# Kernel tuning notes

Hardware: AMD Instinct MI355X
Metric: run time of the kernel (lower is better)

## Reference

```python
import jax, jax.numpy as jnp
import numpy as np

B, C1, D1, C2, D2 = 128, 1152, 8, 10, 16
ROUTING_ITERS = 3


def squash(s, axis=-1, eps=1e-8):
    # squash(s) = (|s|^2 / (1+|s|^2)) * s / sqrt(|s|^2 + eps)
    sq = jnp.sum(s * s, axis=axis, keepdims=True)
    return (sq / (1.0 + sq)) * s / jnp.sqrt(sq + eps)


def setup_inputs() -> dict:
    key = jax.random.key(0)
    k1, k2, k3 = jax.random.split(key, 3)
    inputs = jax.random.normal(k1, (B, C1 * D1), dtype=jnp.float32)
    # W: (caps1, caps2, d2, d1), truncated normal stddev=0.1 (leading batch-1 dim dropped)
    W = jax.random.truncated_normal(k2, -2.0, 2.0, (C1, C2, D2, D1), dtype=jnp.float32) * 0.1
    # routing bias: (1, 1, caps2, d2)
    bias = jax.random.normal(k3, (1, 1, C2, D2), dtype=jnp.float32) * 0.1
    return {"inputs": inputs, "W": W, "bias": bias}


def reference(inputs, W, bias):
    b = inputs.shape[0]
    # PrimaryCaps: reshape to [B, C1, D1] then squash over the capsule dim (axis=-2 of
    # the original [B, C1, 1, D1, 1] tensor == D1 here)
    prim = squash(inputs.reshape(b, C1, D1), axis=-1)
    # DigitalCaps (fast): u_hat[b,i,j,:] = W[i,j] @ prim[b,i]  -> [B, C1, C2, D2]
    u_hat = jnp.einsum('cjdk,bck->bcjd', W, prim)
    u_stop = jax.lax.stop_gradient(u_hat)
    raw = jnp.zeros((b, C1, C2, 1), dtype=inputs.dtype)
    v = None
    for r in range(ROUTING_ITERS):
        u = u_hat if r == ROUTING_ITERS - 1 else u_stop
        c = jax.nn.softmax(raw, axis=2)                      # softmax over output caps
        s = jnp.sum(c * u, axis=1, keepdims=True) + bias     # [B, 1, C2, D2]
        v = squash(s, axis=-1)                               # squash over D2 (orig axis=-2)
        if r != ROUTING_ITERS - 1:
            # agreement: sum over D2 of u * v (v broadcasts over C1)
            raw = raw + jnp.sum(u * v, axis=-1, keepdims=True)
    # original returns [B, 1, C2, D2, 1]
    return v[..., None]
```

## Files before the change

### kernel.cpp

```cpp
#include <hip/hip_runtime.h>
#include <hip/hip_fp16.h>

#define BATCH 128
#define NC1   1152
#define ND1   8
#define NC2   10
#define ND2   16
#define SDIM  (NC2 * ND2)

#define CB 16
#define BB 32

#define NQ   6
#define QCAP (NC1 / NQ)
#define CPGP (QCAP / 32)

__device__ __forceinline__ unsigned pack_h2(float a, float b) {
    __half2 h = __floats2half2_rn(a, b);
    return *reinterpret_cast<unsigned*>(&h);
}
__device__ __forceinline__ float2 unpack_h2(unsigned v) {
    __half2 h = *reinterpret_cast<__half2*>(&v);
    return __half22float2(h);
}
__device__ __forceinline__ unsigned pmul_h2(unsigned a, unsigned b) {
    __half2 ha = *reinterpret_cast<__half2*>(&a);
    __half2 hb = *reinterpret_cast<__half2*>(&b);
    __half2 r = __hmul2(ha, hb);
    return *reinterpret_cast<unsigned*>(&r);
}
__device__ __forceinline__ unsigned padd_h2(unsigned a, unsigned b) {
    __half2 ha = *reinterpret_cast<__half2*>(&a);
    __half2 hb = *reinterpret_cast<__half2*>(&b);
    __half2 r = __hadd2(ha, hb);
    return *reinterpret_cast<unsigned*>(&r);
}

template<int CTRL>
__device__ __forceinline__ unsigned dpp_mov(unsigned v) {
    return (unsigned)__builtin_amdgcn_mov_dpp((int)v, CTRL, 0xF, 0xF, true);
}
__device__ __forceinline__ unsigned row_reduce_h2(unsigned t2) {
    t2 = padd_h2(t2, dpp_mov<0x128>(t2));
    t2 = padd_h2(t2, dpp_mov<0x124>(t2));
    t2 = padd_h2(t2, dpp_mov<0x122>(t2));
    t2 = padd_h2(t2, dpp_mov<0x121>(t2));
    return t2;
}

__global__ void caps_zero(float* __restrict__ s0) {
    s0[blockIdx.x * 256 + threadIdx.x] = 0.0f;
}

__global__ __launch_bounds__(256, 1) void caps_uhat(
    const float* __restrict__ x,
    const float* __restrict__ W,
    unsigned* __restrict__ u_ws,
    float* __restrict__ s0)
{
    const int cb  = blockIdx.x;
    const int bb  = blockIdx.y;
    const int tid = threadIdx.x;
    const int cl  = tid >> 4;
    const int d   = tid & 15;
    const int wl  = tid & 63;

    __shared__ float prim[BB][CB][ND1];

    for (int i = tid; i < BB * CB; i += 256) {
        const int b = i >> 4, c = i & 15;
        const float* xr = x + ((size_t)(bb * BB + b) * NC1 + (cb * CB + c)) * ND1;
        float4 a0 = *(const float4*)(xr);
        float4 a1 = *(const float4*)(xr + 4);
        float sq = a0.x*a0.x + a0.y*a0.y + a0.z*a0.z + a0.w*a0.w
                 + a1.x*a1.x + a1.y*a1.y + a1.z*a1.z + a1.w*a1.w;
        float g = (sq / (1.0f + sq)) * rsqrtf(sq + 1e-8f);
        prim[b][c][0] = a0.x * g; prim[b][c][1] = a0.y * g;
        prim[b][c][2] = a0.z * g; prim[b][c][3] = a0.w * g;
        prim[b][c][4] = a1.x * g; prim[b][c][5] = a1.y * g;
        prim[b][c][6] = a1.z * g; prim[b][c][7] = a1.w * g;
    }
    __syncthreads();

    const int c_glob = cb * CB + cl;
    float w[NC2][ND1];
    #pragma unroll
    for (int j = 0; j < NC2; ++j) {
        const float* Wr = W + (((size_t)c_glob * NC2 + j) * ND2 + d) * ND1;
        float4 w0 = *(const float4*)(Wr);
        float4 w1 = *(const float4*)(Wr + 4);
        w[j][0] = w0.x; w[j][1] = w0.y; w[j][2] = w0.z; w[j][3] = w0.w;
        w[j][4] = w1.x; w[j][5] = w1.y; w[j][6] = w1.z; w[j][7] = w1.w;
    }

    for (int k = 0; k < BB; ++k) {
        const int b = (k + cb) & (BB - 1);
        const int bglob = bb * BB + b;
        float p[ND1];
        #pragma unroll
        for (int kk = 0; kk < ND1; ++kk) p[kk] = prim[b][cl][kk];

        unsigned* ur = u_ws + ((size_t)bglob * 5 * NC1 + c_glob) * 16 + d;
        #pragma unroll
        for (int jp = 0; jp < 5; ++jp) {
            float u0 = 0.f, u1 = 0.f;
            #pragma unroll
            for (int kk = 0; kk < ND1; ++kk) {
                u0 += w[2*jp  ][kk] * p[kk];
                u1 += w[2*jp+1][kk] * p[kk];
            }
            unsigned pk = pack_h2(u0, u1);
            ur[(size_t)jp * (NC1 * 16)] = pk;
            pk = padd_h2(pk, (unsigned)__shfl_xor((int)pk, 16));
            pk = padd_h2(pk, (unsigned)__shfl_xor((int)pk, 32));
            if (wl < 16) {
                float2 f = unpack_h2(pk);
                atomicAdd(&s0[(size_t)bglob * SDIM + (2*jp)   * 16 + d], f.x);
                atomicAdd(&s0[(size_t)bglob * SDIM + (2*jp+1) * 16 + d], f.y);
            }
        }
    }
}

__global__ __launch_bounds__(512, 1) void caps_pass(
    const unsigned* __restrict__ u_ws,
    const float* __restrict__ s0,
    const float* __restrict__ spart_in,
    const float* __restrict__ bias,
    float* __restrict__ spart_out,
    int mode)
{
    const int bx   = blockIdx.x;
    const int b    = bx / NQ;
    const int q    = bx % NQ;
    const int tid  = threadIdx.x;
    const int grp  = tid >> 4;
    const int d    = tid & 15;
    const int wave = tid >> 6;

    __shared__ float vl[SDIM];
    __shared__ float sred[8][SDIM];

    const unsigned* ub = u_ws + (size_t)b * 5 * NC1 * 16 + d;
    const int c0 = q * QCAP + grp;
    unsigned uo[CPGP][5];
    #pragma unroll
    for (int i = 0; i < CPGP; ++i) {
        const int c = c0 + i * 32;
        #pragma unroll
        for (int jp = 0; jp < 5; ++jp)
            uo[i][jp] = ub[(size_t)jp * (NC1 * 16) + (size_t)c * 16];
    }

    if (tid < SDIM) {
        float bv = bias[tid];
        float s_a = 0.1f * s0[(size_t)b * SDIM + tid] + bv;
        float qa = s_a * s_a;
        qa += __shfl_xor(qa, 1); qa += __shfl_xor(qa, 2);
        qa += __shfl_xor(qa, 4); qa += __shfl_xor(qa, 8);
        float v = (qa / (1.0f + qa)) * rsqrtf(qa + 1e-8f) * s_a;
        if (mode == 1) {
            float s_b = bv;
            #pragma unroll
            for (int qq = 0; qq < NQ; ++qq)
                s_b += spart_in[((size_t)b * NQ + qq) * SDIM + tid];
            float qb = s_b * s_b;
            qb += __shfl_xor(qb, 1); qb += __shfl_xor(qb, 2);
            qb += __shfl_xor(qb, 4); qb += __shfl_xor(qb, 8);
            v += (qb / (1.0f + qb)) * rsqrtf(qb + 1e-8f) * s_b;
        }
        vl[tid] = v;
    }
    __syncthreads();

    unsigned vsf[5];
    #pragma unroll
    for (int jp = 0; jp < 5; ++jp)
        vsf[jp] = pack_h2(vl[(2*jp)*16 + d], vl[(2*jp+1)*16 + d]);

    float sp[NC2];
    #pragma unroll
    for (int j = 0; j < NC2; ++j) sp[j] = 0.0f;

    #pragma unroll
    for (int i = 0; i < CPGP; ++i) {
        float u[NC2], r[NC2];
        #pragma unroll
        for (int jp = 0; jp < 5; ++jp) {
            float2 f = unpack_h2(uo[i][jp]);
            u[2*jp] = f.x; u[2*jp+1] = f.y;
            unsigned t2 = row_reduce_h2(pmul_h2(uo[i][jp], vsf[jp]));
            float2 rr = unpack_h2(t2);
            r[2*jp] = rr.x; r[2*jp+1] = rr.y;
        }
        float ssum = 0.0f;
        #pragma unroll
        for (int j = 0; j < NC2; ++j) { r[j] = __expf(r[j]); ssum += r[j]; }
        float inv = 1.0f / ssum;
        #pragma unroll
        for (int j = 0; j < NC2; ++j) sp[j] += (r[j] * inv) * u[j];
    }

    #pragma unroll
    for (int j = 0; j < NC2; ++j) {
        sp[j] += __shfl_xor(sp[j], 16);
        sp[j] += __shfl_xor(sp[j], 32);
    }
    if ((tid & 63) < 16) {
        #pragma unroll
        for (int j = 0; j < NC2; ++j) sred[wave][j * 16 + d] = sp[j];
    }
    __syncthreads();
    if (tid < SDIM) {
        float acc = 0.0f;
        #pragma unroll
        for (int w = 0; w < 8; ++w) acc += sred[w][tid];
        spart_out[((size_t)b * NQ + q) * SDIM + tid] = acc;
    }
}

__global__ void caps_comb2(const float* __restrict__ spart,
                           const float* __restrict__ bias,
                           float* __restrict__ out) {
    const int b = blockIdx.x, tid = threadIdx.x;
    if (tid >= SDIM) return;
    float s = bias[tid];
    #pragma unroll
    for (int q = 0; q < NQ; ++q)
        s += spart[((size_t)b * NQ + q) * SDIM + tid];
    float sq = s * s;
    sq += __shfl_xor(sq, 1); sq += __shfl_xor(sq, 2);
    sq += __shfl_xor(sq, 4); sq += __shfl_xor(sq, 8);
    out[(size_t)b * SDIM + tid] = (sq / (1.0f + sq)) * rsqrtf(sq + 1e-8f) * s;
}

__global__ __launch_bounds__(1024) void caps_fused(
    const float* __restrict__ x, const float* __restrict__ W,
    const float* __restrict__ bias, float* __restrict__ out)
{
    const int b    = blockIdx.x;
    const int tid  = threadIdx.x;
    const int grp  = tid >> 4;
    const int d    = tid & 15;
    const int wave = tid >> 6;
    const int lane = tid & 63;

    __shared__ float prim[NC1][ND1];
    __shared__ float sred[16][SDIM];
    __shared__ float vbuf[SDIM];

    const float* xb = x + (size_t)b * (NC1 * ND1);
    for (int c = tid; c < NC1; c += 1024) {
        float4 a0 = *(const float4*)(xb + c * 8);
        float4 a1 = *(const float4*)(xb + c * 8 + 4);
        float sq = a0.x*a0.x + a0.y*a0.y + a0.z*a0.z + a0.w*a0.w
                 + a1.x*a1.x + a1.y*a1.y + a1.z*a1.z + a1.w*a1.w;
        float g = (sq / (1.0f + sq)) * rsqrtf(sq + 1e-8f);
        prim[c][0] = a0.x * g; prim[c][1] = a0.y * g;
        prim[c][2] = a0.z * g; prim[c][3] = a0.w * g;
        prim[c][4] = a1.x * g; prim[c][5] = a1.y * g;
        prim[c][6] = a1.z * g; prim[c][7] = a1.w * g;
    }
    __syncthreads();

    float vsum[NC2], sp[NC2];
    for (int pass = 0; pass < 3; ++pass) {
        #pragma unroll
        for (int j = 0; j < NC2; ++j) sp[j] = 0.0f;
        for (int c = grp; c < NC1; c += 64) {
            float p[8];
            #pragma unroll
            for (int k = 0; k < 8; ++k) p[k] = prim[c][k];
            const float* Wc = W + (size_t)c * (NC2 * ND2 * ND1) + d * ND1;
            float u[NC2];
            #pragma unroll
            for (int j = 0; j < NC2; ++j) {
                const float4 w0 = *(const float4*)(Wc + j * (ND2 * ND1));
                const float4 w1 = *(const float4*)(Wc + j * (ND2 * ND1) + 4);
                u[j] = w0.x*p[0] + w0.y*p[1] + w0.z*p[2] + w0.w*p[3]
                     + w1.x*p[4] + w1.y*p[5] + w1.z*p[6] + w1.w*p[7];
            }
            if (pass == 0) {
                #pragma unroll
                for (int j = 0; j < NC2; ++j) sp[j] += u[j];
            } else {
                float r[NC2];
                #pragma unroll
                for (int j = 0; j < NC2; ++j) {
                    float t = u[j] * vsum[j];
                    t += __shfl_xor(t, 1); t += __shfl_xor(t, 2);
                    t += __shfl_xor(t, 4); t += __shfl_xor(t, 8);
                    r[j] = t;
                }
                float m = r[0];
                #pragma unroll
                for (int j = 1; j < NC2; ++j) m = fmaxf(m, r[j]);
                float ssum = 0.0f;
                #pragma unroll
                for (int j = 0; j < NC2; ++j) { r[j] = __expf(r[j] - m); ssum += r[j]; }
                float inv = 1.0f / ssum;
                #pragma unroll
                for (int j = 0; j < NC2; ++j) sp[j] += (r[j] * inv) * u[j];
            }
        }
        #pragma unroll
        for (int j = 0; j < NC2; ++j) {
            sp[j] += __shfl_xor(sp[j], 16);
            sp[j] += __shfl_xor(sp[j], 32);
        }
        if (lane < 16) {
            #pragma unroll
            for (int j = 0; j < NC2; ++j) sred[wave][j * 16 + d] = sp[j];
        }
        __syncthreads();
        if (tid < SDIM) {
            float acc = 0.0f;
            #pragma unroll
            for (int w = 0; w < 16; ++w) acc += sred[w][tid];
            float s = bias[tid] + (pass == 0 ? 0.1f * acc : acc);
            float sq = s * s;
            sq += __shfl_xor(sq, 1); sq += __shfl_xor(sq, 2);
            sq += __shfl_xor(sq, 4); sq += __shfl_xor(sq, 8);
            float vv = (sq / (1.0f + sq)) * rsqrtf(sq + 1e-8f) * s;
            if (pass == 2) out[(size_t)b * SDIM + tid] = vv;
            else           vbuf[tid] = vv;
        }
        __syncthreads();
        if (pass < 2) {
            #pragma unroll
            for (int j = 0; j < NC2; ++j) {
                float vv = vbuf[j * 16 + d];
                vsum[j] = (pass == 0) ? vv : (vsum[j] + vv);
            }
        }
        __syncthreads();
    }
}

extern "C" void kernel_launch(void* const* d_in, const int* in_sizes, int n_in,
                              void* d_out, int out_size, void* d_ws, size_t ws_size,
                              hipStream_t stream) {
    const float* x    = (const float*)d_in[0];
    const float* W    = (const float*)d_in[1];
    const float* bias = (const float*)d_in[2];
    float* out = (float*)d_out;

    const size_t u_bytes  = (size_t)BATCH * 5 * NC1 * 16 * 4;
    const size_t s0_bytes = (size_t)BATCH * SDIM * 4;
    const size_t sp_bytes = (size_t)BATCH * NQ * SDIM * 4;
    const size_t need = u_bytes + s0_bytes + 2 * sp_bytes;

    if (ws_size >= need) {
        unsigned* u_ws  = (unsigned*)d_ws;
        float*    s0    = (float*)((char*)d_ws + u_bytes);
        float*    sp1   = (float*)((char*)d_ws + u_bytes + s0_bytes);
        float*    sp2   = (float*)((char*)d_ws + u_bytes + s0_bytes + sp_bytes);

        caps_zero <<<80, 256, 0, stream>>>(s0);
        caps_uhat <<<dim3(NC1 / CB, BATCH / BB), 256, 0, stream>>>(x, W, u_ws, s0);
        caps_pass <<<BATCH * NQ, 512, 0, stream>>>(u_ws, s0, sp1, bias, sp1, 0);
        caps_pass <<<BATCH * NQ, 512, 0, stream>>>(u_ws, s0, sp1, bias, sp2, 1);
        caps_comb2<<<BATCH, 192, 0, stream>>>(sp2, bias, out);
    } else {
        caps_fused<<<BATCH, 1024, 0, stream>>>(x, W, bias, out);
    }
}
```

Measured before the change: 72.26 us.

## Replace s0 atomics with per-wave partial buffer and separate reduction kernel

```diff
diff --git a/kernel.cpp b/kernel.cpp
--- a/kernel.cpp
+++ b/kernel.cpp
@@ -7,13 +7,13 @@
 #define NC2   10
 #define ND2   16
 #define SDIM  (NC2 * ND2)
+#define NP    288
 
 #define CB 16
 #define BB 32
 
-#define NQ   6
+#define NQ   4
 #define QCAP (NC1 / NQ)
-#define CPGP (QCAP / 32)
 
 __device__ __forceinline__ unsigned pack_h2(float a, float b) {
     __half2 h = __floats2half2_rn(a, b);
@@ -48,15 +48,11 @@
     return t2;
 }
 
-__global__ void caps_zero(float* __restrict__ s0) {
-    s0[blockIdx.x * 256 + threadIdx.x] = 0.0f;
-}
-
 __global__ __launch_bounds__(256, 1) void caps_uhat(
     const float* __restrict__ x,
     const float* __restrict__ W,
     unsigned* __restrict__ u_ws,
-    float* __restrict__ s0)
+    unsigned* __restrict__ s0p)
 {
     const int cb  = blockIdx.x;
     const int bb  = blockIdx.y;
@@ -64,6 +60,7 @@
     const int cl  = tid >> 4;
     const int d   = tid & 15;
     const int wl  = tid & 63;
+    const int wv  = tid >> 6;
 
     __shared__ float prim[BB][CB][ND1];
 
@@ -93,33 +90,64 @@
         w[j][4] = w1.x; w[j][5] = w1.y; w[j][6] = w1.z; w[j][7] = w1.w;
     }
 
-    for (int k = 0; k < BB; ++k) {
-        const int b = (k + cb) & (BB - 1);
-        const int bglob = bb * BB + b;
-        float p[ND1];
-        #pragma unroll
-        for (int kk = 0; kk < ND1; ++kk) p[kk] = prim[b][cl][kk];
-
-        unsigned* ur = u_ws + ((size_t)bglob * 5 * NC1 + c_glob) * 16 + d;
+    const int pid = cb * 4 + wv;
+
+    for (int k = 0; k < BB; k += 2) {
+        const int b0 = (k + cb) & (BB - 1);
+        const int b1 = (k + 1 + cb) & (BB - 1);
+        const int g0 = bb * BB + b0;
+        const int g1 = bb * BB + b1;
+
+        float p0[ND1], p1[ND1];
+        #pragma unroll
+        for (int kk = 0; kk < ND1; ++kk) { p0[kk] = prim[b0][cl][kk];
+                                           p1[kk] = prim[b1][cl][kk]; }
+
+        unsigned* ur0 = u_ws + ((size_t)g0 * 5 * NC1 + c_glob) * 16 + d;
+        unsigned* ur1 = u_ws + ((size_t)g1 * 5 * NC1 + c_glob) * 16 + d;
+        unsigned* q0  = s0p + ((size_t)g0 * NP + pid) * 80 + d;
+        unsigned* q1  = s0p + ((size_t)g1 * NP + pid) * 80 + d;
+
         #pragma unroll
         for (int jp = 0; jp < 5; ++jp) {
-            float u0 = 0.f, u1 = 0.f;
+            float u00 = 0.f, u01 = 0.f, u10 = 0.f, u11 = 0.f;
             #pragma unroll
             for (int kk = 0; kk < ND1; ++kk) {
-                u0 += w[2*jp  ][kk] * p[kk];
-                u1 += w[2*jp+1][kk] * p[kk];
+                u00 += w[2*jp  ][kk] * p0[kk];
+                u01 += w[2*jp+1][kk] * p0[kk];
+                u10 += w[2*jp  ][kk] * p1[kk];
+                u11 += w[2*jp+1][kk] * p1[kk];
             }
-            unsigned pk = pack_h2(u0, u1);
-            ur[(size_t)jp * (NC1 * 16)] = pk;
-            pk = padd_h2(pk, (unsigned)__shfl_xor((int)pk, 16));
-            pk = padd_h2(pk, (unsigned)__shfl_xor((int)pk, 32));
+            unsigned pk0 = pack_h2(u00, u01);
+            unsigned pk1 = pack_h2(u10, u11);
+            ur0[(size_t)jp * (NC1 * 16)] = pk0;
+            ur1[(size_t)jp * (NC1 * 16)] = pk1;
+            pk0 = padd_h2(pk0, (unsigned)__shfl_xor((int)pk0, 16));
+            pk0 = padd_h2(pk0, (unsigned)__shfl_xor((int)pk0, 32));
+            pk1 = padd_h2(pk1, (unsigned)__shfl_xor((int)pk1, 16));
+            pk1 = padd_h2(pk1, (unsigned)__shfl_xor((int)pk1, 32));
             if (wl < 16) {
-                float2 f = unpack_h2(pk);
-                atomicAdd(&s0[(size_t)bglob * SDIM + (2*jp)   * 16 + d], f.x);
-                atomicAdd(&s0[(size_t)bglob * SDIM + (2*jp+1) * 16 + d], f.y);
+                q0[jp * 16] = pk0;
+                q1[jp * 16] = pk1;
             }
         }
     }
+}
+
+__global__ void caps_s0sum(const unsigned* __restrict__ s0p,
+                           float* __restrict__ s0) {
+    const int b = blockIdx.x, tid = threadIdx.x;
+    if (tid >= 80) return;
+    const unsigned* base = s0p + (size_t)b * NP * 80 + tid;
+    float sx = 0.f, sy = 0.f;
+    #pragma unroll 4
+    for (int p = 0; p < NP; ++p) {
+        float2 f = unpack_h2(base[(size_t)p * 80]);
+        sx += f.x; sy += f.y;
+    }
+    const int jp = tid >> 4, d = tid & 15;
+    s0[(size_t)b * SDIM + jp * 32 + d]      = sx;
+    s0[(size_t)b * SDIM + jp * 32 + 16 + d] = sy;
 }
 
 __global__ __launch_bounds__(512, 1) void caps_pass(
@@ -131,8 +159,8 @@
     int mode)
 {
     const int bx   = blockIdx.x;
-    const int b    = bx / NQ;
-    const int q    = bx % NQ;
+    const int b    = bx >> 2;
+    const int q    = bx & 3;
     const int tid  = threadIdx.x;
     const int grp  = tid >> 4;
     const int d    = tid & 15;
@@ -140,17 +168,6 @@
 
     __shared__ float vl[SDIM];
     __shared__ float sred[8][SDIM];
-
-    const unsigned* ub = u_ws + (size_t)b * 5 * NC1 * 16 + d;
-    const int c0 = q * QCAP + grp;
-    unsigned uo[CPGP][5];
-    #pragma unroll
-    for (int i = 0; i < CPGP; ++i) {
-        const int c = c0 + i * 32;
-        #pragma unroll
-        for (int jp = 0; jp < 5; ++jp)
-            uo[i][jp] = ub[(size_t)jp * (NC1 * 16) + (size_t)c * 16];
-    }
 
     if (tid < SDIM) {
         float bv = bias[tid];
@@ -178,18 +195,31 @@
     for (int jp = 0; jp < 5; ++jp)
         vsf[jp] = pack_h2(vl[(2*jp)*16 + d], vl[(2*jp+1)*16 + d]);
 
+    const unsigned* ub = u_ws + (size_t)b * 5 * NC1 * 16 + d;
+    const int c0 = q * QCAP + grp;
+
     float sp[NC2];
     #pragma unroll
     for (int j = 0; j < NC2; ++j) sp[j] = 0.0f;
 
-    #pragma unroll
-    for (int i = 0; i < CPGP; ++i) {
+    unsigned o[5], on[5];
+    #pragma unroll
+    for (int jp = 0; jp < 5; ++jp)
+        o[jp] = ub[(size_t)jp * (NC1 * 16) + (size_t)c0 * 16];
+
+    for (int i = 0; i < 9; ++i) {
+        if (i + 1 < 9) {
+            const int c = c0 + (i + 1) * 32;
+            #pragma unroll
+            for (int jp = 0; jp < 5; ++jp)
+                on[jp] = ub[(size_t)jp * (NC1 * 16) + (size_t)c * 16];
+        }
         float u[NC2], r[NC2];
         #pragma unroll
         for (int jp = 0; jp < 5; ++jp) {
-            float2 f = unpack_h2(uo[i][jp]);
+            float2 f = unpack_h2(o[jp]);
             u[2*jp] = f.x; u[2*jp+1] = f.y;
-            unsigned t2 = row_reduce_h2(pmul_h2(uo[i][jp], vsf[jp]));
+            unsigned t2 = row_reduce_h2(pmul_h2(o[jp], vsf[jp]));
             float2 rr = unpack_h2(t2);
             r[2*jp] = rr.x; r[2*jp+1] = rr.y;
         }
@@ -199,6 +229,8 @@
         float inv = 1.0f / ssum;
         #pragma unroll
         for (int j = 0; j < NC2; ++j) sp[j] += (r[j] * inv) * u[j];
+        #pragma unroll
+        for (int jp = 0; jp < 5; ++jp) o[jp] = on[jp];
     }
 
     #pragma unroll
@@ -345,19 +377,22 @@
     const float* bias = (const float*)d_in[2];
     float* out = (float*)d_out;
 
-    const size_t u_bytes  = (size_t)BATCH * 5 * NC1 * 16 * 4;
-    const size_t s0_bytes = (size_t)BATCH * SDIM * 4;
-    const size_t sp_bytes = (size_t)BATCH * NQ * SDIM * 4;
-    const size_t need = u_bytes + s0_bytes + 2 * sp_bytes;
+    const size_t u_bytes   = (size_t)BATCH * 5 * NC1 * 16 * 4;
+    const size_t s0p_bytes = (size_t)BATCH * NP * 80 * 4;
+    const size_t s0_bytes  = (size_t)BATCH * SDIM * 4;
+    const size_t sp_bytes  = (size_t)BATCH * NQ * SDIM * 4;
+    const size_t need = u_bytes + s0p_bytes + s0_bytes + 2 * sp_bytes;
 
     if (ws_size >= need) {
-        unsigned* u_ws  = (unsigned*)d_ws;
-        float*    s0    = (float*)((char*)d_ws + u_bytes);
-        float*    sp1   = (float*)((char*)d_ws + u_bytes + s0_bytes);
-        float*    sp2   = (float*)((char*)d_ws + u_bytes + s0_bytes + sp_bytes);
-
-        caps_zero <<<80, 256, 0, stream>>>(s0);
-        caps_uhat <<<dim3(NC1 / CB, BATCH / BB), 256, 0, stream>>>(x, W, u_ws, s0);
+        char* p = (char*)d_ws;
+        unsigned* u_ws = (unsigned*)p;                    p += u_bytes;
+        unsigned* s0p  = (unsigned*)p;                    p += s0p_bytes;
+        float*    s0   = (float*)p;                       p += s0_bytes;
+        float*    sp1  = (float*)p;                       p += sp_bytes;
+        float*    sp2  = (float*)p;
+
+        caps_uhat <<<dim3(NC1 / CB, BATCH / BB), 256, 0, stream>>>(x, W, u_ws, s0p);
+        caps_s0sum<<<BATCH, 128, 0, stream>>>(s0p, s0);
         caps_pass <<<BATCH * NQ, 512, 0, stream>>>(u_ws, s0, sp1, bias, sp1, 0);
         caps_pass <<<BATCH * NQ, 512, 0, stream>>>(u_ws, s0, sp1, bias, sp2, 1);
         caps_comb2<<<BATCH, 192, 0, stream>>>(sp2, bias, out);
```

After: 76.79 us. 1.06x slower.
